# Optimization experiments

Hardware: AMD Instinct MI355X
Metric: run time of the kernel (lower is better)

Reference implementation:

```python
import jax, jax.numpy as jnp
import numpy as np
from jax import lax

B, T, D = 256, 512, 256          # batch, time, input_dim (neurons)
HE, HC, HG = 256, 256, 256       # encoder/controller/generator hidden
L, F = 64, 64                    # latent_dim, factor_dim


def gru_cell(x, h, Wih, Whh, bih, bhh):
    # PyTorch GRU gate order: r, z, n
    gi = x @ Wih.T + bih
    gh = h @ Whh.T + bhh
    ir, iz, inn = jnp.split(gi, 3, axis=-1)
    hr, hz, hn = jnp.split(gh, 3, axis=-1)
    r = jax.nn.sigmoid(ir + hr)
    z = jax.nn.sigmoid(iz + hz)
    n = jnp.tanh(inn + r * hn)
    return (1.0 - z) * n + z * h


def setup_inputs() -> dict:
    key = jax.random.key(0)
    ks = iter(jax.random.split(key, 40))
    def p(shape, scale=0.05):
        return (jax.random.normal(next(ks), shape, dtype=jnp.float32) * scale)
    inp = {
        "x": jax.random.normal(next(ks), (B, T, D), dtype=jnp.float32),
        "eps_u": jax.random.normal(next(ks), (T, B, L), dtype=jnp.float32),
        # bidirectional encoder GRU (forward / backward directions)
        "Wih_ef": p((3 * HE, D)), "Whh_ef": p((3 * HE, HE)), "bih_ef": p((3 * HE,)), "bhh_ef": p((3 * HE,)),
        "Wih_eb": p((3 * HE, D)), "Whh_eb": p((3 * HE, HE)), "bih_eb": p((3 * HE,)), "bhh_eb": p((3 * HE,)),
        # initial-condition heads
        "W_mu0": p((L, 2 * HE)), "b_mu0": p((L,)), "W_lv0": p((L, 2 * HE)), "b_lv0": p((L,)),
        # controller GRU + heads
        "Wih_c": p((3 * HC, D + F)), "Whh_c": p((3 * HC, HC)), "bih_c": p((3 * HC,)), "bhh_c": p((3 * HC,)),
        "W_cmu": p((L, HC)), "b_cmu": p((L,)), "W_clv": p((L, HC)), "b_clv": p((L,)),
        # generator GRU
        "Wih_g": p((3 * HG, L)), "Whh_g": p((3 * HG, HG)), "bih_g": p((3 * HG,)), "bhh_g": p((3 * HG,)),
        # readouts
        "W_f": p((F, HG)), "b_f": p((F,)), "W_r": p((D, F)), "b_r": p((D,)),
    }
    return inp


def reference(x, eps_u, Wih_ef, Whh_ef, bih_ef, bhh_ef, Wih_eb, Whh_eb, bih_eb, bhh_eb,
              W_mu0, b_mu0, W_lv0, b_lv0, Wih_c, Whh_c, bih_c, bhh_c,
              W_cmu, b_cmu, W_clv, b_clv, Wih_g, Whh_g, bih_g, bhh_g,
              W_f, b_f, W_r, b_r):
    xt = jnp.transpose(x, (1, 0, 2))  # [T, B, D]
    h0 = jnp.zeros((x.shape[0], HE), dtype=x.dtype)

    def enc_f(h, x_t):
        return gru_cell(x_t, h, Wih_ef, Whh_ef, bih_ef, bhh_ef), None

    def enc_b(h, x_t):
        return gru_cell(x_t, h, Wih_eb, Whh_eb, bih_eb, bhh_eb), None

    h_fwd, _ = lax.scan(enc_f, h0, xt)
    h_bwd, _ = lax.scan(enc_b, h0, xt, reverse=True)
    h_enc = jnp.concatenate([h_fwd, h_bwd], axis=-1)  # [B, 2*HE]

    mu0 = h_enc @ W_mu0.T + b_mu0
    lv0 = h_enc @ W_lv0.T + b_lv0
    kl_ics = (0.5 * jnp.sum(jnp.exp(lv0) + mu0 ** 2 - 1.0 - lv0, axis=1)).mean()
    # note: z0 is sampled in the original but never used (generator starts from zeros)

    c0 = jnp.zeros((x.shape[0], HC), dtype=x.dtype)
    g0 = jnp.zeros((x.shape[0], HG), dtype=x.dtype)
    f0 = jnp.zeros((x.shape[0], F), dtype=x.dtype)

    def step(carry, inputs):
        c_h, g_h, prev_f = carry
        x_t, eps_t = inputs
        c_in = jnp.concatenate([x_t, prev_f], axis=-1)  # [B, D+F]
        c_h = gru_cell(c_in, c_h, Wih_c, Whh_c, bih_c, bhh_c)
        mu_u = c_h @ W_cmu.T + b_cmu
        lv_u = c_h @ W_clv.T + b_clv
        u_t = mu_u + eps_t * jnp.exp(0.5 * lv_u)
        kl_t = (0.5 * jnp.sum(jnp.exp(lv_u) + mu_u ** 2 - 1.0 - lv_u, axis=1)).mean()
        g_h = gru_cell(u_t, g_h, Wih_g, Whh_g, bih_g, bhh_g)
        factors = g_h @ W_f.T + b_f
        rates_t = jnp.exp(factors @ W_r.T + b_r)
        return (c_h, g_h, factors), (rates_t, factors, kl_t)

    _, (rates, factors_all, kl_ts) = lax.scan(step, (c0, g0, f0), (xt, eps_u))
    rates = jnp.transpose(rates, (1, 0, 2))           # [B, T, D]
    factors_all = jnp.transpose(factors_all, (1, 0, 2))  # [B, T, F]
    kl_ctrl = kl_ts.mean()  # sum of per-step means / T
    return (rates, kl_ics, kl_ctrl, factors_all)
```

## Files before the change

### kernel.cpp

```cpp
#include <hip/hip_runtime.h>

typedef unsigned char u8;
typedef unsigned short u16;
typedef unsigned int u32;
typedef unsigned long long u64;
typedef short short8 __attribute__((ext_vector_type(8)));
typedef __bf16 bf16x8 __attribute__((ext_vector_type(8)));
typedef float f32x4 __attribute__((ext_vector_type(4)));
typedef float f32x2 __attribute__((ext_vector_type(2)));
typedef long longx2 __attribute__((ext_vector_type(2)));

#define DEV static __device__ __forceinline__

struct Params {
  const float *x, *eps;
  const float *Wih_ef, *Whh_ef, *bih_ef, *bhh_ef;
  const float *Wih_eb, *Whh_eb, *bih_eb, *bhh_eb;
  const float *W_mu0, *b_mu0, *W_lv0, *b_lv0;
  const float *Wih_c, *Whh_c, *bih_c, *bhh_c;
  const float *W_cmu, *b_cmu, *W_clv, *b_clv;
  const float *Wih_g, *Whh_g, *bih_g, *bhh_g;
  const float *W_f, *b_f, *W_r, *b_r;
  u8  *Xf8;
  u16 *ebf;
  u16 *wihcbf, *wihefbf, *wihebbf;
  float *bfc;
  float *bfe;
  u8 *wihef8, *whhef8, *wiheb8, *whheb8;
  u8 *whhc8, *whhg8;
  u8 *wihcf8, *wihg8;
  u8 *wf8, *wcmu8, *wclv8;
  u16 *wrbf;
  float *cbn;
  float *ebn;
  float *gb;
  float *hdb;
  float *fb2;
  float *eb;
  float *henc;
  float *klacc;
  float *klics;
  u8 *Gxc;
  u8 *Gxe;
  int useGxe;
  float *out;
};

constexpr size_t RATES_N = 33554432ull;
constexpr size_t FOUT    = RATES_N + 2ull;
constexpr size_t GXE_D   = 100663296ull;

DEV u16 f2bf(float x) {
  unsigned u = __builtin_bit_cast(unsigned, x);
  u = (u + 0x7FFFu + ((u >> 16) & 1u)) >> 16;
  return (u16)u;
}
DEV float bf2f(u32 s) { return __builtin_bit_cast(float, s << 16); }
DEV unsigned f2e4m3(float x) {
  unsigned u = __builtin_bit_cast(unsigned, x);
  unsigned s = (u >> 24) & 0x80u;
  float ax = __builtin_bit_cast(float, u & 0x7FFFFFFFu);
  if (ax > 448.f) return s | 0x7E;
  if (ax < 0.0009765625f) return s;
  if (ax < 0.015625f) {
    int m = (int)rintf(ax * 512.f);
    if (m >= 8) return s | 0x08;
    return s | (unsigned)m;
  }
  unsigned au = __builtin_bit_cast(unsigned, ax);
  int E = (int)(au >> 23) - 127;
  unsigned m = au & 0x7FFFFFu;
  unsigned r = (m + 0x7FFFFu + ((m >> 20) & 1u)) >> 20;
  if (r >= 8) { r = 0; ++E; if (E > 8) return s | 0x7E; }
  return s | ((unsigned)(E + 7) << 3) | r;
}
DEV float e4m3tof(unsigned b) {
  unsigned s = (b & 0x80u) << 24;
  unsigned e = (b >> 3) & 15u, m = b & 7u;
  float v;
  if (e) v = __builtin_bit_cast(float, ((e + 120u) << 23) | (m << 20));
  else   v = (float)m * 0.001953125f;
  return __builtin_bit_cast(float, __builtin_bit_cast(unsigned, v) | s);
}
template <bool HI>
DEV unsigned pk2fp8(float a, float b, unsigned old) {
#if __has_builtin(__builtin_amdgcn_cvt_pk_fp8_f32)
  return (unsigned)__builtin_amdgcn_cvt_pk_fp8_f32(a, b, (int)old, HI);
#else
  unsigned p = f2e4m3(a) | (f2e4m3(b) << 8);
  return HI ? ((old & 0xFFFFu) | (p << 16)) : ((old & 0xFFFF0000u) | p);
#endif
}
template <bool HI>
DEV f32x2 pkf32(unsigned w) {
#if __has_builtin(__builtin_amdgcn_cvt_pk_f32_fp8)
  return __builtin_amdgcn_cvt_pk_f32_fp8((int)w, HI);
#else
  unsigned h = HI ? (w >> 16) : w;
  f32x2 r; r[0] = e4m3tof(h & 255u); r[1] = e4m3tof((h >> 8) & 255u); return r;
#endif
}
DEV float sigm(float x) { return 1.f / (1.f + __expf(-x)); }
DEV float ftanh(float x) { float t = __expf(2.f * x); return 1.f - 2.f / (t + 1.f); }
DEV float gru_h(float pr, float pz, float pin, float phn, float hp) {
  float r = sigm(pr), z = sigm(pz);
  float n = ftanh(pin + r * phn);
  return (1.f - z) * n + z * hp;
}
DEV u64 pack8f8(const float* s) {
  u64 p = 0;
  #pragma unroll
  for (int e = 0; e < 8; ++e) p |= (u64)f2e4m3(s[e]) << (8 * e);
  return p;
}

DEV f32x4 MFMA(short8 a, short8 b, f32x4 c) {
  return __builtin_amdgcn_mfma_f32_16x16x32_bf16(
      __builtin_bit_cast(bf16x8, a), __builtin_bit_cast(bf16x8, b), c, 0, 0, 0);
}
DEV f32x4 mfma8(long a, long b, f32x4 c) {
  return __builtin_amdgcn_mfma_f32_16x16x32_fp8_fp8(a, b, c, 0, 0, 0);
}
DEV short8 ldfrag(const u16* p0, int stride) {
  const int l = threadIdx.x & 63;
  const u16* p = p0 + (size_t)(l & 15) * stride + ((l >> 4) << 3);
  return *reinterpret_cast<const short8*>(p);
}
DEV short8 ldfrag_f32(const float* p0, int stride) {
  const int l = threadIdx.x & 63;
  const float* p = p0 + (size_t)(l & 15) * stride + ((l >> 4) << 3);
  f32x4 a = *reinterpret_cast<const f32x4*>(p);
  f32x4 b = *reinterpret_cast<const f32x4*>(p + 4);
  short8 r;
  r[0]=(short)f2bf(a[0]); r[1]=(short)f2bf(a[1]); r[2]=(short)f2bf(a[2]); r[3]=(short)f2bf(a[3]);
  r[4]=(short)f2bf(b[0]); r[5]=(short)f2bf(b[1]); r[6]=(short)f2bf(b[2]); r[7]=(short)f2bf(b[3]);
  return r;
}
DEV longx2 ldws2(const u8* w, int tile, int p) {
  return *(const longx2*)(w + ((size_t)tile << 12) + (p << 10) + ((threadIdx.x & 63) << 4));
}
DEV longx2 ldws64x(const u8* w, int tile) {
  return *(const longx2*)(w + ((size_t)tile << 10) + ((threadIdx.x & 63) << 4));
}
DEV int fragoff(int row, int jb) { return jb * 128 + ((row ^ (jb & 15)) << 3); }
DEV long ldsF(const u8* m, int kk) {
  int l = threadIdx.x & 63;
  int jb = kk * 4 + (l >> 4);
  return *(const long*)(m + fragoff(l & 15, jb));
}
DEV long ldsF64(const u8* m, int k2) {
  int l = threadIdx.x & 63;
  int jb = k2 * 4 + (l >> 4);
  return *(const long*)(m + fragoff(l & 15, jb));
}
DEV void stF(u8* m, int row, int col, unsigned v) {
  *(unsigned*)(m + fragoff(row, col >> 3) + (col & 7)) = v;
}
DEV short8 ldsB16(const u8* m, int r0, int kk) {
  int l = threadIdx.x & 63;
  int row = r0 + (l & 15);
  int off = row * 512 + kk * 64 + ((l >> 4) << 4);
  off ^= (row & 7) << 4;
  return *(const short8*)(m + off);
}
DEV void stage16(u8* dst, const u8* src, int nbytes) {
  for (int i = threadIdx.x * 16; i < nbytes; i += blockDim.x * 16) {
    int row = i >> 9;
    int off = i ^ ((row & 7) << 4);
    *(f32x4*)(dst + off) = *(const f32x4*)(src + i);
  }
}
DEV void stageLin(u8* dst, const u8* src, int nbytes) {
  for (int i = threadIdx.x * 16; i < nbytes; i += 512 * 16)
    *(f32x4*)(dst + i) = *(const f32x4*)(src + i);
}

__global__ __launch_bounds__(256) void k_init(Params P) {
  const size_t g  = (size_t)blockIdx.x * 256 + threadIdx.x;
  const size_t gs = (size_t)gridDim.x * 256;
  if (!P.useGxe) {
    for (size_t i = g; i < 4194304ull; i += gs) {
      size_t flat = i << 3;
      int b = (int)(flat >> 17);
      int rem = (int)(flat & 131071);
      int t = rem >> 8, d = rem & 255;
      *(u64*)(P.Xf8 + (((size_t)t * 256 + b) << 8) + d) = pack8f8(P.x + flat);
    }
  }
  for (size_t o = g; o < 1048576ull; o += gs) {
    int l = (int)(o & 63), k2 = (int)((o >> 6) & 1);
    int bt = (int)((o >> 7) & 15), t = (int)(o >> 11);
    int row = bt * 16 + (l & 15), col = k2 * 32 + ((l >> 4) << 3);
    const float* s = P.eps + ((size_t)t * 256 + row) * 64 + col;
    f32x4 v0 = *(const f32x4*)s, v1 = *(const f32x4*)(s + 4);
    short8 ob;
    ob[0]=(short)f2bf(v0[0]); ob[1]=(short)f2bf(v0[1]); ob[2]=(short)f2bf(v0[2]); ob[3]=(short)f2bf(v0[3]);
    ob[4]=(short)f2bf(v1[0]); ob[5]=(short)f2bf(v1[1]); ob[6]=(short)f2bf(v1[2]); ob[7]=(short)f2bf(v1[3]);
    *(short8*)((u8*)P.ebf + o * 16) = ob;
  }
  const int gi = (int)g, gsi = (int)gs;
  for (int i = gi; i < 24576; i += gsi) {
    int l = i & 63, kk = (i >> 6) & 7, tile = i >> 9;
    int row = tile * 16 + (l & 15), col = kk * 32 + ((l >> 4) << 3);
    size_t so = (size_t)row * 256 + col;
    size_t db = ((size_t)tile << 12) + ((kk >> 1) << 10) + (l << 4) + ((kk & 1) << 3);
    *(u64*)(P.whhc8  + db) = pack8f8(P.Whh_c  + so);
    *(u64*)(P.whhg8  + db) = pack8f8(P.Whh_g  + so);
    *(u64*)(P.wihef8 + db) = pack8f8(P.Wih_ef + so);
    *(u64*)(P.whhef8 + db) = pack8f8(P.Whh_ef + so);
    *(u64*)(P.wiheb8 + db) = pack8f8(P.Wih_eb + so);
    *(u64*)(P.whheb8 + db) = pack8f8(P.Whh_eb + so);
  }
  for (int i = gi; i < 2048; i += gsi) {
    int l = i & 63, kk = (i >> 6) & 7, tile = i >> 9;
    int row = tile * 16 + (l & 15), col = kk * 32 + ((l >> 4) << 3);
    size_t so = (size_t)row * 256 + col;
    size_t db = ((size_t)tile << 12) + ((kk >> 1) << 10) + (l << 4) + ((kk & 1) << 3);
    *(u64*)(P.wf8   + db) = pack8f8(P.W_f   + so);
    *(u64*)(P.wcmu8 + db) = pack8f8(P.W_cmu + so);
    *(u64*)(P.wclv8 + db) = pack8f8(P.W_clv + so);
  }
  for (int i = gi; i < 6144; i += gsi) {
    int l = i & 63, k2 = (i >> 6) & 1, tile = i >> 7;
    int row = tile * 16 + (l & 15), col = k2 * 32 + ((l >> 4) << 3);
    size_t db = ((size_t)tile << 10) + (l << 4) + (k2 << 3);
    *(u64*)(P.wihcf8 + db) = pack8f8(P.Wih_c + (size_t)row * 320 + 256 + col);
    *(u64*)(P.wihg8  + db) = pack8f8(P.Wih_g + (size_t)row * 64 + col);
  }
  for (int i = gi; i < 196608; i += gsi) {
    int r = i >> 8, c = i & 255;
    P.wihcbf[i]  = f2bf(P.Wih_c[r * 320 + c]);
    P.wihefbf[i] = f2bf(P.Wih_ef[i]);
    P.wihebbf[i] = f2bf(P.Wih_eb[i]);
  }
  for (int i = gi; i < 16384; i += gsi) P.wrbf[i] = f2bf(P.W_r[i]);
  for (int i = gi; i < 768; i += gsi) {
    P.bfc[i] = P.bih_c[i] + (i < 512 ? P.bhh_c[i] : 0.f);
    P.bfe[i]       = P.bih_ef[i] + (i < 512 ? P.bhh_ef[i] : 0.f);
    P.bfe[768 + i] = P.bih_eb[i] + (i < 512 ? P.bhh_eb[i] : 0.f);
  }
  for (int i = gi; i < 256; i += gsi) {
    P.cbn[i] = P.bhh_c[512 + i];
    P.ebn[i]       = P.bhh_ef[512 + i];
    P.ebn[256 + i] = P.bhh_eb[512 + i];
    P.gb[i]        = P.bih_g[i] + P.bhh_g[i];
    P.gb[256 + i]  = P.bih_g[256 + i] + P.bhh_g[256 + i];
    P.gb[512 + i]  = P.bih_g[512 + i];
    P.gb[768 + i]  = P.bhh_g[512 + i];
    P.eb[i]        = P.bih_ef[i] + P.bhh_ef[i];
    P.eb[256 + i]  = P.bih_ef[256 + i] + P.bhh_ef[256 + i];
    P.eb[512 + i]  = P.bih_ef[512 + i];
    P.eb[768 + i]  = P.bhh_ef[512 + i];
    P.eb[1024 + i] = P.bih_eb[i] + P.bhh_eb[i];
    P.eb[1280 + i] = P.bih_eb[256 + i] + P.bhh_eb[256 + i];
    P.eb[1536 + i] = P.bih_eb[512 + i];
    P.eb[1792 + i] = P.bhh_eb[512 + i];
  }
  for (int i = gi; i < 128; i += gsi) P.hdb[i] = (i < 64) ? P.b_cmu[i] : P.b_clv[i - 64];
  for (int i = gi; i < 64; i += gsi)  P.fb2[i] = P.b_f[i];
}

__global__ __launch_bounds__(512, 2) void k_gx(Params P) {
  extern __shared__ char smem[];
  u8* sA = (u8*)smem;
  u8* sB = sA + 65536;
  const int nc = blockIdx.x % 6;
  const int tb = blockIdx.x / 6;
  const int t = tb >> 1, bh = tb & 1;
  for (int i = threadIdx.x * 8; i < 32768; i += 512 * 8) {
    int r = i >> 8, c = i & 255;
    const float* s = P.x + ((size_t)(bh * 128 + r) * 512 + t) * 256 + c;
    f32x4 v0 = *(const f32x4*)s, v1 = *(const f32x4*)(s + 4);
    short8 o;
    o[0]=(short)f2bf(v0[0]); o[1]=(short)f2bf(v0[1]); o[2]=(short)f2bf(v0[2]); o[3]=(short)f2bf(v0[3]);
    o[4]=(short)f2bf(v1[0]); o[5]=(short)f2bf(v1[1]); o[6]=(short)f2bf(v1[2]); o[7]=(short)f2bf(v1[3]);
    int off = (r * 512 + c * 2) ^ ((r & 7) << 4);
    *(short8*)(sB + off) = o;
  }
  const int lane = threadIdx.x & 63, wid = threadIdx.x >> 6;
  const int rq = (lane >> 4) << 2;
  const int nglob = nc * 128 + wid * 16;
  const int nmm = P.useGxe ? 3 : 1;
  #pragma unroll 1
  for (int mm = 0; mm < nmm; ++mm) {
    const u16* Abf = (mm == 0) ? P.wihcbf : ((mm == 1) ? P.wihefbf : P.wihebbf);
    const float* bias = (mm == 0) ? P.bfc : (P.bfe + (mm - 1) * 768);
    u8* dst = (mm == 0) ? P.Gxc : (P.Gxe + (size_t)(mm - 1) * GXE_D);
    stage16(sA, (const u8*)(Abf + (size_t)nc * 128 * 256), 65536);
    __syncthreads();
    short8 Af[8];
    #pragma unroll
    for (int kk = 0; kk < 8; ++kk) Af[kk] = ldsB16(sA, wid * 16, kk);
    float bq[4];
    #pragma unroll
    for (int q = 0; q < 4; ++q) bq[q] = bias[nglob + rq + q];
    #pragma unroll 1
    for (int bt = 0; bt < 8; ++bt) {
      f32x4 acc = {0.f, 0.f, 0.f, 0.f};
      #pragma unroll
      for (int kk = 0; kk < 8; ++kk)
        acc = MFMA(Af[kk], ldsB16(sB, bt * 16, kk), acc);
      float v0 = acc[0] + bq[0], v1 = acc[1] + bq[1], v2 = acc[2] + bq[2], v3 = acc[3] + bq[3];
      unsigned pw = pk2fp8<false>(v0, v1, 0u); pw = pk2fp8<true>(v2, v3, pw);
      *(u32*)(dst + (((size_t)(t * 16 + bh * 8 + bt) * 48 + (nglob >> 4)) << 8) + (lane << 2)) = pw;
    }
    __syncthreads();
  }
}

DEV void cg_role(const Params& P, int blk, char* smem) {
  u8* sWcf = (u8*)smem;
  u8* sWg  = sWcf + 49152;
  u8* sWhd = sWg + 49152;
  u8* hc8  = sWhd + 32768;
  u8* hg8  = hc8 + 8192;
  u8* f8b  = hg8 + 8192;
  float* sml  = (float*)(f8b + 2048);
  float* sred = sml + 16 * 132;

  const int lane = threadIdx.x & 63, wid = threadIdx.x >> 6;
  const int cl = lane & 15, rq = (lane >> 4) << 2;
  const int b0 = blk << 4, j0 = wid << 5, jt = wid << 1;
  const int sel = wid >> 2, l0 = (wid & 3) << 4;

  stageLin(sWcf, P.wihcf8, 49152);
  stageLin(sWg,  P.wihg8,  49152);
  stageLin(sWhd, P.wcmu8, 16384);
  stageLin(sWhd + 16384, P.wclv8, 16384);
  for (int i = threadIdx.x * 4; i < 18432; i += 512 * 4) *(int*)(hc8 + i) = 0;

  f32x4 bnv[2], brv[2], bzv[2], biv[2], bhv2[2];
  #pragma unroll
  for (int c2 = 0; c2 < 2; ++c2) {
    int j = j0 + c2 * 16 + rq;
    bnv[c2]  = *(const f32x4*)(P.cbn + j);
    brv[c2]  = *(const f32x4*)(P.gb + j);
    bzv[c2]  = *(const f32x4*)(P.gb + 256 + j);
    biv[c2]  = *(const f32x4*)(P.gb + 512 + j);
    bhv2[c2] = *(const f32x4*)(P.gb + 768 + j);
  }
  f32x4 hbv = *(const f32x4*)(P.hdb + sel * 64 + l0 + rq);
  f32x4 fbv = {0, 0, 0, 0};
  if (wid < 4) fbv = *(const f32x4*)(P.fb2 + (wid << 4) + rq);

  f32x4 hcM[2] = {{0,0,0,0},{0,0,0,0}};
  f32x4 hgM[2] = {{0,0,0,0},{0,0,0,0}};
  float klv = 0.f;
  __syncthreads();

  #pragma unroll 1
  for (int t = 0; t < 512; ++t) {
    const int cur = t & 1, prv = cur ^ 1;
    u8 *hcP = hc8 + prv * 4096, *hcC = hc8 + cur * 4096;
    u8 *hgP = hg8 + prv * 4096, *hgC = hg8 + cur * 4096;
    u32 gx[6];
    { const u8* gp = P.Gxc + (((size_t)(t * 16 + blk) * 48) << 8) + (lane << 2);
      #pragma unroll
      for (int c2 = 0; c2 < 2; ++c2)
        #pragma unroll
        for (int g3 = 0; g3 < 3; ++g3)
          gx[c2 * 3 + g3] = *(const u32*)(gp + ((g3 * 16 + jt + c2) << 8));
    }
    short8 ee0 = *(const short8*)((const u8*)P.ebf + (((size_t)(t * 16 + blk) * 2 + 0) << 10) + lane * 16);
    short8 ee1 = *(const short8*)((const u8*)P.ebf + (((size_t)(t * 16 + blk) * 2 + 1) << 10) + lane * 16);
    long hf[8];
    #pragma unroll
    for (int kk = 0; kk < 8; ++kk) hf[kk] = ldsF(hcP, kk);
    long ff0 = ldsF64(f8b + prv * 1024, 0);
    long ff1 = ldsF64(f8b + prv * 1024, 1);
    #pragma unroll
    for (int c2 = 0; c2 < 2; ++c2) {
      longx2 w0[4], w1[4], w2[4];
      #pragma unroll
      for (int p = 0; p < 4; ++p) {
        w0[p] = ldws2(P.whhc8,      jt + c2, p);
        w1[p] = ldws2(P.whhc8, 16 + jt + c2, p);
        w2[p] = ldws2(P.whhc8, 32 + jt + c2, p);
      }
      longx2 cf0 = ldws64x(sWcf,      jt + c2);
      longx2 cf1 = ldws64x(sWcf, 16 + jt + c2);
      longx2 cf2 = ldws64x(sWcf, 32 + jt + c2);
      f32x4 ar = {0,0,0,0}, az = {0,0,0,0}, ai = {0,0,0,0}, ah = {0,0,0,0};
      #pragma unroll
      for (int p = 0; p < 4; ++p) {
        ar = mfma8(w0[p].x, hf[2*p], ar);  ar = mfma8(w0[p].y, hf[2*p+1], ar);
        az = mfma8(w1[p].x, hf[2*p], az);  az = mfma8(w1[p].y, hf[2*p+1], az);
        ah = mfma8(w2[p].x, hf[2*p], ah);  ah = mfma8(w2[p].y, hf[2*p+1], ah);
      }
      ar = mfma8(cf0.x, ff0, ar); ar = mfma8(cf0.y, ff1, ar);
      az = mfma8(cf1.x, ff0, az); az = mfma8(cf1.y, ff1, az);
      ai = mfma8(cf2.x, ff0, ai); ai = mfma8(cf2.y, ff1, ai);
      f32x2 rlo = pkf32<false>(gx[c2*3+0]), rhi = pkf32<true>(gx[c2*3+0]);
      f32x2 zlo = pkf32<false>(gx[c2*3+1]), zhi = pkf32<true>(gx[c2*3+1]);
      f32x2 nlo = pkf32<false>(gx[c2*3+2]), nhi = pkf32<true>(gx[c2*3+2]);
      f32x4 bn = bnv[c2];
      float h0 = gru_h(ar[0]+rlo[0], az[0]+zlo[0], ai[0]+nlo[0], ah[0]+bn[0], hcM[c2][0]);
      float h1 = gru_h(ar[1]+rlo[1], az[1]+zlo[1], ai[1]+nlo[1], ah[1]+bn[1], hcM[c2][1]);
      float h2 = gru_h(ar[2]+rhi[0], az[2]+zhi[0], ai[2]+nhi[0], ah[2]+bn[2], hcM[c2][2]);
      float h3 = gru_h(ar[3]+rhi[1], az[3]+zhi[1], ai[3]+nhi[1], ah[3]+bn[3], hcM[c2][3]);
      hcM[c2][0] = h0; hcM[c2][1] = h1; hcM[c2][2] = h2; hcM[c2][3] = h3;
      unsigned pw = pk2fp8<false>(h0, h1, 0u); pw = pk2fp8<true>(h2, h3, pw);
      stF(hcC, cl, j0 + c2 * 16 + rq, pw);
    }
    longx2 pg0[4], pg1[4], pg2[4];
    #pragma unroll
    for (int p = 0; p < 4; ++p) {
      pg0[p] = ldws2(P.whhg8,      jt, p);
      pg1[p] = ldws2(P.whhg8, 16 + jt, p);
      pg2[p] = ldws2(P.whhg8, 32 + jt, p);
    }
    __syncthreads();
    { long hcv[8];
      #pragma unroll
      for (int kk = 0; kk < 8; ++kk) hcv[kk] = ldsF(hcC, kk);
      f32x4 am = {0,0,0,0};
      #pragma unroll
      for (int p = 0; p < 4; ++p) {
        longx2 wp = ldws2(sWhd + sel * 16384, wid & 3, p);
        am = mfma8(wp.x, hcv[2*p], am);
        am = mfma8(wp.y, hcv[2*p+1], am);
      }
      am += hbv;
      *(f32x4*)(sml + cl * 132 + sel * 64 + l0 + rq) = am;
    }
    __syncthreads();
    long U[2];
    { const float* ml = sml + cl * 132;
      const int kh = (lane >> 4) << 3;
      #pragma unroll
      for (int k2 = 0; k2 < 2; ++k2) {
        f32x4 mu0 = *(const f32x4*)(ml + k2 * 32 + kh);
        f32x4 mu1 = *(const f32x4*)(ml + k2 * 32 + kh + 4);
        f32x4 lv0 = *(const f32x4*)(ml + 64 + k2 * 32 + kh);
        f32x4 lv1 = *(const f32x4*)(ml + 64 + k2 * 32 + kh + 4);
        short8 ev = k2 ? ee1 : ee0;
        float uu[8];
        #pragma unroll
        for (int e = 0; e < 4; ++e) {
          float epv = bf2f((u32)(u16)ev[e]);
          uu[e] = mu0[e] + epv * __expf(0.5f * lv0[e]);
        }
        #pragma unroll
        for (int e = 0; e < 4; ++e) {
          float epv = bf2f((u32)(u16)ev[4 + e]);
          uu[4 + e] = mu1[e] + epv * __expf(0.5f * lv1[e]);
        }
        unsigned pa = pk2fp8<false>(uu[0], uu[1], 0u); pa = pk2fp8<true>(uu[2], uu[3], pa);
        unsigned pb = pk2fp8<false>(uu[4], uu[5], 0u); pb = pk2fp8<true>(uu[6], uu[7], pb);
        U[k2] = (long)(((u64)pb << 32) | (u64)pa);
      }
    }
    long hg[8];
    #pragma unroll
    for (int kk = 0; kk < 8; ++kk) hg[kk] = ldsF(hgP, kk);
    #pragma unroll
    for (int c2 = 0; c2 < 2; ++c2) {
      longx2 g0[4], g1[4], g2[4];
      if (c2 == 0) {
        #pragma unroll
        for (int p = 0; p < 4; ++p) { g0[p] = pg0[p]; g1[p] = pg1[p]; g2[p] = pg2[p]; }
      } else {
        #pragma unroll
        for (int p = 0; p < 4; ++p) {
          g0[p] = ldws2(P.whhg8,      jt + 1, p);
          g1[p] = ldws2(P.whhg8, 16 + jt + 1, p);
          g2[p] = ldws2(P.whhg8, 32 + jt + 1, p);
        }
      }
      longx2 u0 = ldws64x(sWg,      jt + c2);
      longx2 u1 = ldws64x(sWg, 16 + jt + c2);
      longx2 u2 = ldws64x(sWg, 32 + jt + c2);
      f32x4 gr = {0,0,0,0}, gz = {0,0,0,0}, gi = {0,0,0,0}, gh = {0,0,0,0};
      #pragma unroll
      for (int p = 0; p < 4; ++p) {
        gr = mfma8(g0[p].x, hg[2*p], gr);  gr = mfma8(g0[p].y, hg[2*p+1], gr);
        gz = mfma8(g1[p].x, hg[2*p], gz);  gz = mfma8(g1[p].y, hg[2*p+1], gz);
        gh = mfma8(g2[p].x, hg[2*p], gh);  gh = mfma8(g2[p].y, hg[2*p+1], gh);
      }
      gr = mfma8(u0.x, U[0], gr); gr = mfma8(u0.y, U[1], gr);
      gz = mfma8(u1.x, U[0], gz); gz = mfma8(u1.y, U[1], gz);
      gi = mfma8(u2.x, U[0], gi); gi = mfma8(u2.y, U[1], gi);
      float h0 = gru_h(gr[0]+brv[c2][0], gz[0]+bzv[c2][0], gi[0]+biv[c2][0], gh[0]+bhv2[c2][0], hgM[c2][0]);
      float h1 = gru_h(gr[1]+brv[c2][1], gz[1]+bzv[c2][1], gi[1]+biv[c2][1], gh[1]+bhv2[c2][1], hgM[c2][1]);
      float h2 = gru_h(gr[2]+brv[c2][2], gz[2]+bzv[c2][2], gi[2]+biv[c2][2], gh[2]+bhv2[c2][2], hgM[c2][2]);
      float h3 = gru_h(gr[3]+brv[c2][3], gz[3]+bzv[c2][3], gi[3]+biv[c2][3], gh[3]+bhv2[c2][3], hgM[c2][3]);
      hgM[c2][0] = h0; hgM[c2][1] = h1; hgM[c2][2] = h2; hgM[c2][3] = h3;
      unsigned pw = pk2fp8<false>(h0, h1, 0u); pw = pk2fp8<true>(h2, h3, pw);
      stF(hgC, cl, j0 + c2 * 16 + rq, pw);
    }
    __syncthreads();
    if (wid < 4) {
      long hgv[8];
      #pragma unroll
      for (int kk = 0; kk < 8; ++kk) hgv[kk] = ldsF(hgC, kk);
      f32x4 af = {0,0,0,0};
      #pragma unroll
      for (int p = 0; p < 4; ++p) {
        longx2 wp = ldws2(P.wf8, wid, p);
        af = mfma8(wp.x, hgv[2*p], af);
        af = mfma8(wp.y, hgv[2*p+1], af);
      }
      af += fbv;
      float* fo = P.out + FOUT + (size_t)(b0 + cl) * 32768 + (size_t)t * 64 + wid * 16 + rq;
      f32x2 lo = {af[0], af[1]}, hi2 = {af[2], af[3]};
      *(f32x2*)fo = lo;
      *(f32x2*)(fo + 2) = hi2;
      unsigned pw = pk2fp8<false>(af[0], af[1], 0u); pw = pk2fp8<true>(af[2], af[3], pw);
      stF(f8b + cur * 1024, cl, wid * 16 + rq, pw);
    } else {
      #pragma unroll
      for (int e = 0; e < 4; ++e) {
        int p = ((wid - 4) * 64 + lane) * 4 + e;
        int row = p >> 6, l = p & 63;
        float mu = sml[row * 132 + l], lv = sml[row * 132 + 64 + l];
        klv += __expf(lv) + mu * mu - 1.f - lv;
      }
    }
    __syncthreads();
  }
  if (wid >= 4) {
    float v = klv;
    v += __shfl_down(v, 32); v += __shfl_down(v, 16); v += __shfl_down(v, 8);
    v += __shfl_down(v, 4);  v += __shfl_down(v, 2);  v += __shfl_down(v, 1);
    if (lane == 0) sred[wid] = v;
  }
  __syncthreads();
  if (threadIdx.x == 0) P.klacc[blk] = sred[4] + sred[5] + sred[6] + sred[7];
}

template <bool GXE>
DEV void enc_role(const Params& P, int dir, int b0, char* smem) {
  u8* sWhh = (u8*)smem;
  u8* h8   = sWhh + 131072;
  u8* sx   = h8 + 8192;
  const int lane = threadIdx.x & 63, wid = threadIdx.x >> 6;
  const int cl = lane & 15, rq = (lane >> 4) << 2;
  const int j0 = wid << 5, jt = wid << 1;
  const int btile = b0 >> 4;
  const u8* wihG = dir ? P.wiheb8 : P.wihef8;
  const u8* whhG = dir ? P.whheb8 : P.whhef8;
  stageLin(sWhh, whhG, 131072);
  for (int i = threadIdx.x * 4; i < 8192; i += 512 * 4) *(int*)(h8 + i) = 0;
  f32x4 bnv[2], brv[2], bzv[2], biv[2], bhv2[2];
  #pragma unroll
  for (int c2 = 0; c2 < 2; ++c2) {
    int j = j0 + c2 * 16 + rq;
    if (GXE) {
      bnv[c2] = *(const f32x4*)(P.ebn + dir * 256 + j);
    } else {
      const float* ebt = P.eb + dir * 1024;
      brv[c2]  = *(const f32x4*)(ebt + j);
      bzv[c2]  = *(const f32x4*)(ebt + 256 + j);
      biv[c2]  = *(const f32x4*)(ebt + 512 + j);
      bhv2[c2] = *(const f32x4*)(ebt + 768 + j);
    }
  }
  f32x4 heM[2] = {{0,0,0,0},{0,0,0,0}};
  const int ssrc = threadIdx.x * 8;
  if (!GXE) {
    const int t0 = dir ? 511 : 0;
    *(u64*)(sx + fragoff(threadIdx.x >> 5, threadIdx.x & 31)) =
        *(const u64*)(P.Xf8 + (((size_t)t0 * 256 + b0) << 8) + ssrc);
  }
  __syncthreads();

  #pragma unroll 1
  for (int i = 0; i < 512; ++i) {
    const int cur = i & 1, prv = cur ^ 1;
    const int t = dir ? (511 - i) : i;
    u8 *hP = h8 + prv * 4096, *hC = h8 + cur * 4096;
    u32 gx[6];
    u64 xpre = 0;
    const u8* sxc = sx + cur * 4096;
    if (GXE) {
      const u8* gp = P.Gxe + (size_t)dir * GXE_D +
                     (((size_t)(t * 16 + btile) * 48) << 8) + (lane << 2);
      #pragma unroll
      for (int c2 = 0; c2 < 2; ++c2)
        #pragma unroll
        for (int g3 = 0; g3 < 3; ++g3)
          gx[c2 * 3 + g3] = *(const u32*)(gp + ((g3 * 16 + jt + c2) << 8));
    } else {
      if (i < 511) {
        int tn = dir ? (t - 1) : (t + 1);
        xpre = *(const u64*)(P.Xf8 + (((size_t)tn * 256 + b0) << 8) + ssrc);
      }
    }
    long hp[8];
    #pragma unroll
    for (int kk = 0; kk < 8; ++kk) hp[kk] = ldsF(hP, kk);
    #pragma unroll
    for (int c2 = 0; c2 < 2; ++c2) {
      longx2 Hr[4], Hz[4], Hn[4];
      #pragma unroll
      for (int p = 0; p < 4; ++p) {
        Hr[p] = ldws2(sWhh,      jt + c2, p);
        Hz[p] = ldws2(sWhh, 16 + jt + c2, p);
        Hn[p] = ldws2(whhG, 32 + jt + c2, p);
      }
      f32x4 er = {0,0,0,0}, ez = {0,0,0,0}, ei = {0,0,0,0}, eh = {0,0,0,0};
      #pragma unroll
      for (int p = 0; p < 4; ++p) {
        er = mfma8(Hr[p].x, hp[2*p], er);  er = mfma8(Hr[p].y, hp[2*p+1], er);
        ez = mfma8(Hz[p].x, hp[2*p], ez);  ez = mfma8(Hz[p].y, hp[2*p+1], ez);
        eh = mfma8(Hn[p].x, hp[2*p], eh);  eh = mfma8(Hn[p].y, hp[2*p+1], eh);
      }
      if (!GXE) {
        long xv[8];
        #pragma unroll
        for (int kk = 0; kk < 8; ++kk) xv[kk] = ldsF(sxc, kk);
        longx2 Ir[4], Iz[4], In[4];
        #pragma unroll
        for (int p = 0; p < 4; ++p) {
          Ir[p] = ldws2(wihG,      jt + c2, p);
          Iz[p] = ldws2(wihG, 16 + jt + c2, p);
          In[p] = ldws2(wihG, 32 + jt + c2, p);
        }
        #pragma unroll
        for (int p = 0; p < 4; ++p) {
          er = mfma8(Ir[p].x, xv[2*p], er);  er = mfma8(Ir[p].y, xv[2*p+1], er);
          ez = mfma8(Iz[p].x, xv[2*p], ez);  ez = mfma8(Iz[p].y, xv[2*p+1], ez);
          ei = mfma8(In[p].x, xv[2*p], ei);  ei = mfma8(In[p].y, xv[2*p+1], ei);
        }
      }
      float h0, h1, h2, h3;
      if (GXE) {
        f32x2 rlo = pkf32<false>(gx[c2*3+0]), rhi = pkf32<true>(gx[c2*3+0]);
        f32x2 zlo = pkf32<false>(gx[c2*3+1]), zhi = pkf32<true>(gx[c2*3+1]);
        f32x2 nlo = pkf32<false>(gx[c2*3+2]), nhi = pkf32<true>(gx[c2*3+2]);
        f32x4 bn = bnv[c2];
        h0 = gru_h(er[0]+rlo[0], ez[0]+zlo[0], nlo[0], eh[0]+bn[0], heM[c2][0]);
        h1 = gru_h(er[1]+rlo[1], ez[1]+zlo[1], nlo[1], eh[1]+bn[1], heM[c2][1]);
        h2 = gru_h(er[2]+rhi[0], ez[2]+zhi[0], nhi[0], eh[2]+bn[2], heM[c2][2]);
        h3 = gru_h(er[3]+rhi[1], ez[3]+zhi[1], nhi[1], eh[3]+bn[3], heM[c2][3]);
      } else {
        h0 = gru_h(er[0]+brv[c2][0], ez[0]+bzv[c2][0], ei[0]+biv[c2][0], eh[0]+bhv2[c2][0], heM[c2][0]);
        h1 = gru_h(er[1]+brv[c2][1], ez[1]+bzv[c2][1], ei[1]+biv[c2][1], eh[1]+bhv2[c2][1], heM[c2][1]);
        h2 = gru_h(er[2]+brv[c2][2], ez[2]+bzv[c2][2], ei[2]+biv[c2][2], eh[2]+bhv2[c2][2], heM[c2][2]);
        h3 = gru_h(er[3]+brv[c2][3], ez[3]+bzv[c2][3], ei[3]+biv[c2][3], eh[3]+bhv2[c2][3], heM[c2][3]);
      }
      heM[c2][0] = h0; heM[c2][1] = h1; heM[c2][2] = h2; heM[c2][3] = h3;
      unsigned pw = pk2fp8<false>(h0, h1, 0u); pw = pk2fp8<true>(h2, h3, pw);
      stF(hC, cl, j0 + c2 * 16 + rq, pw);
    }
    if (!GXE && i < 511)
      *(u64*)(sx + prv * 4096 + fragoff(threadIdx.x >> 5, threadIdx.x & 31)) = xpre;
    __syncthreads();
  }
  #pragma unroll
  for (int c2 = 0; c2 < 2; ++c2)
    *(f32x4*)(P.henc + (size_t)(dir * 256 + b0 + cl) * 256 + j0 + c2 * 16 + rq) = heM[c2];
}

__global__ __launch_bounds__(512)
__attribute__((amdgpu_waves_per_eu(2, 2)))
void k_main(Params P) {
  extern __shared__ char smem[];
  const int blk = blockIdx.x;
  if (blk < 16) cg_role(P, blk, smem);
  else {
    const int e = blk - 16;
    if (P.useGxe) enc_role<true>(P, e >> 4, (e & 15) << 4, smem);
    else          enc_role<false>(P, e >> 4, (e & 15) << 4, smem);
  }
}

__global__ __launch_bounds__(256) void k_post(Params P) {
  const int blk = blockIdx.x;
  if (blk < 32) {
    __shared__ float red[4];
    float ka = 0.f;
    #pragma unroll 1
    for (int pp = 0; pp < 2; ++pp) {
      int p = blk * 512 + threadIdx.x * 2 + pp;
      int b = p >> 6, l = p & 63;
      float mu = P.b_mu0[l], lv = P.b_lv0[l];
      const float* wm = P.W_mu0 + (size_t)l * 512;
      const float* wl = P.W_lv0 + (size_t)l * 512;
      const float* h0 = P.henc + (size_t)b * 256;
      const float* h1 = P.henc + (size_t)(256 + b) * 256;
      #pragma unroll 4
      for (int k = 0; k < 256; ++k) {
        float hf = h0[k], hb = h1[k];
        mu += hf * wm[k] + hb * wm[256 + k];
        lv += hf * wl[k] + hb * wl[256 + k];
      }
      ka += __expf(lv) + mu * mu - 1.f - lv;
    }
    const int lane = threadIdx.x & 63, wid = threadIdx.x >> 6;
    ka += __shfl_down(ka, 32); ka += __shfl_down(ka, 16); ka += __shfl_down(ka, 8);
    ka += __shfl_down(ka, 4);  ka += __shfl_down(ka, 2);  ka += __shfl_down(ka, 1);
    if (lane == 0) red[wid] = ka;
    __syncthreads();
    if (threadIdx.x == 0) P.klics[blk] = red[0] + red[1] + red[2] + red[3];
  } else {
    const int lane = threadIdx.x & 63, wid = threadIdx.x >> 6;
    const int cl = lane & 15, rq = (lane >> 4) << 2;
    const int gw = (blk - 32) * 4 + wid;
    const size_t r0 = (size_t)gw << 4;
    const float* Fs = P.out + FOUT;
    short8 F0 = ldfrag_f32(Fs + r0 * 64, 64);
    short8 F1 = ldfrag_f32(Fs + r0 * 64 + 32, 64);
    #pragma unroll 1
    for (int ct = 0; ct < 16; ++ct) {
      const int d0 = ct << 4;
      const u16* W = P.wrbf + (size_t)d0 * 64;
      f32x4 a = {0,0,0,0};
      a = MFMA(ldfrag(W, 64), F0, a);
      a = MFMA(ldfrag(W + 32, 64), F1, a);
      f32x4 rb = *(const f32x4*)(P.b_r + d0 + rq);
      f32x4 o;
      o[0] = __expf(a[0] + rb[0]); o[1] = __expf(a[1] + rb[1]);
      o[2] = __expf(a[2] + rb[2]); o[3] = __expf(a[3] + rb[3]);
      *(f32x4*)(P.out + (r0 + cl) * 256 + d0 + rq) = o;
    }
  }
}

__global__ void k_final(Params P) {
  if (threadIdx.x == 0) {
    float s = 0.f, s2 = 0.f;
    for (int i = 0; i < 16; ++i) s += P.klacc[i];
    for (int i = 0; i < 32; ++i) s2 += P.klics[i];
    P.out[RATES_N]     = s2 * (0.5f / 256.f);
    P.out[RATES_N + 1] = s  * (0.5f / (256.f * 512.f));
  }
}

extern "C" void kernel_launch(void* const* d_in, const int* in_sizes, int n_in,
                              void* d_out, int out_size, void* d_ws, size_t ws_size,
                              hipStream_t stream) {
  (void)in_sizes; (void)n_in; (void)out_size;
  Params P;
  const float* const* in = (const float* const*)d_in;
  P.x = in[0];      P.eps = in[1];
  P.Wih_ef = in[2]; P.Whh_ef = in[3]; P.bih_ef = in[4]; P.bhh_ef = in[5];
  P.Wih_eb = in[6]; P.Whh_eb = in[7]; P.bih_eb = in[8]; P.bhh_eb = in[9];
  P.W_mu0 = in[10]; P.b_mu0 = in[11]; P.W_lv0 = in[12]; P.b_lv0 = in[13];
  P.Wih_c = in[14]; P.Whh_c = in[15]; P.bih_c = in[16]; P.bhh_c = in[17];
  P.W_cmu = in[18]; P.b_cmu = in[19]; P.W_clv = in[20]; P.b_clv = in[21];
  P.Wih_g = in[22]; P.Whh_g = in[23]; P.bih_g = in[24]; P.bhh_g = in[25];
  P.W_f = in[26];   P.b_f = in[27];   P.W_r = in[28];   P.b_r = in[29];

  char* w = (char*)d_ws;
  size_t off = 0;
  auto take = [&](size_t bytes) -> char* {
    char* r = w + off;
    off = (off + bytes + 255) & ~(size_t)255;
    return r;
  };
  P.Xf8     = (u8*)take(33554432ull);
  P.ebf     = (u16*)take(16777216ull * 2);
  P.wihcbf  = (u16*)take(196608ull * 2);
  P.wihefbf = (u16*)take(196608ull * 2);
  P.wihebbf = (u16*)take(196608ull * 2);
  P.bfc     = (float*)take(768ull * 4);
  P.bfe     = (float*)take(1536ull * 4);
  P.wihef8  = (u8*)take(196608ull);
  P.whhef8  = (u8*)take(196608ull);
  P.wiheb8  = (u8*)take(196608ull);
  P.whheb8  = (u8*)take(196608ull);
  P.whhc8   = (u8*)take(196608ull);
  P.whhg8   = (u8*)take(196608ull);
  P.wihcf8  = (u8*)take(49152ull);
  P.wihg8   = (u8*)take(49152ull);
  P.wf8     = (u8*)take(16384ull);
  P.wcmu8   = (u8*)take(16384ull);
  P.wclv8   = (u8*)take(16384ull);
  P.wrbf    = (u16*)take(16384ull * 2);
  P.cbn     = (float*)take(256ull * 4);
  P.ebn     = (float*)take(512ull * 4);
  P.gb      = (float*)take(1024ull * 4);
  P.hdb     = (float*)take(128ull * 4);
  P.fb2     = (float*)take(64ull * 4);
  P.eb      = (float*)take(2048ull * 4);
  P.henc    = (float*)take(131072ull * 4);
  P.klacc   = (float*)take(64ull * 4);
  P.klics   = (float*)take(64ull * 4);
  size_t gxe_off = (off + 255) & ~(size_t)255;
  P.useGxe = (gxe_off + 2 * GXE_D <= ws_size) ? 1 : 0;
  P.Gxe = P.useGxe ? (u8*)(w + gxe_off) : (u8*)w;
  P.Gxc = (u8*)d_out;
  P.out = (float*)d_out;

  hipLaunchKernelGGL(k_init,  dim3(2048), dim3(256), 0, stream, P);
  hipLaunchKernelGGL(k_gx,    dim3(6144), dim3(512), 131072, stream, P);
  hipLaunchKernelGGL(k_main,  dim3(48),   dim3(512), 158016, stream, P);
  hipLaunchKernelGGL(k_post,  dim3(2080), dim3(256), 0, stream, P);
  hipLaunchKernelGGL(k_final, dim3(1),    dim3(64),  0, stream, P);
}
```

Measured before the change: 4.644 ms.

## Fold factor readout into controller input weights to drop per-step sync

Precomputes Wih_c[:,256:] @ W_f (and its bias term) so the controller GRU consumes the previous generator hidden state directly instead of the previous factors. The factors buffer in shared memory and the trailing barrier in the recurrent loop go away, which shortens the serial per-step dependency chain. In exchange the controller does a K=256 fp8 matmul against a 196KB global weight instead of a K=64 matmul from shared memory, and the fused product is quantized to fp8, which changes rounding.

```diff
diff --git a/kernel.cpp b/kernel.cpp
--- a/kernel.cpp
+++ b/kernel.cpp
@@ -28,9 +28,11 @@
   float *bfe;
   u8 *wihef8, *whhef8, *wiheb8, *whheb8;
   u8 *whhc8, *whhg8;
-  u8 *wihcf8, *wihg8;
+  u8 *wcomb8;
+  u8 *wihg8;
   u8 *wf8, *wcmu8, *wclv8;
   u16 *wrbf;
+  float *foldc;
   float *cbn;
   float *ebn;
   float *gb;
@@ -148,11 +150,6 @@
   int jb = kk * 4 + (l >> 4);
   return *(const long*)(m + fragoff(l & 15, jb));
 }
-DEV long ldsF64(const u8* m, int k2) {
-  int l = threadIdx.x & 63;
-  int jb = k2 * 4 + (l >> 4);
-  return *(const long*)(m + fragoff(l & 15, jb));
-}
 DEV void stF(u8* m, int row, int col, unsigned v) {
   *(unsigned*)(m + fragoff(row, col >> 3) + (col & 7)) = v;
 }
@@ -211,6 +208,24 @@
     *(u64*)(P.wiheb8 + db) = pack8f8(P.Wih_eb + so);
     *(u64*)(P.whheb8 + db) = pack8f8(P.Whh_eb + so);
   }
+  for (int i = gi; i < 196608; i += gsi) {
+    int r = i >> 8, c = i & 255;
+    float acc = 0.f;
+    const float* wr = P.Wih_c + (size_t)r * 320 + 256;
+    #pragma unroll 4
+    for (int l = 0; l < 64; ++l) acc += wr[l] * P.W_f[l * 256 + c];
+    int tile = r >> 4, row15 = r & 15;
+    int kk = c >> 5, lh = (c >> 3) & 3, e = c & 7;
+    int lane = lh * 16 + row15;
+    size_t db = ((size_t)tile << 12) + ((size_t)(kk >> 1) << 10) + (lane << 4) + ((kk & 1) << 3) + e;
+    P.wcomb8[db] = (u8)f2e4m3(acc);
+  }
+  for (int i = gi; i < 768; i += gsi) {
+    float acc = 0.f;
+    const float* wr = P.Wih_c + (size_t)i * 320 + 256;
+    for (int l = 0; l < 64; ++l) acc += wr[l] * P.b_f[l];
+    P.foldc[i] = acc;
+  }
   for (int i = gi; i < 2048; i += gsi) {
     int l = i & 63, kk = (i >> 6) & 7, tile = i >> 9;
     int row = tile * 16 + (l & 15), col = kk * 32 + ((l >> 4) << 3);
@@ -224,7 +239,6 @@
     int l = i & 63, k2 = (i >> 6) & 1, tile = i >> 7;
     int row = tile * 16 + (l & 15), col = k2 * 32 + ((l >> 4) << 3);
     size_t db = ((size_t)tile << 10) + (l << 4) + (k2 << 3);
-    *(u64*)(P.wihcf8 + db) = pack8f8(P.Wih_c + (size_t)row * 320 + 256 + col);
     *(u64*)(P.wihg8  + db) = pack8f8(P.Wih_g + (size_t)row * 64 + col);
   }
   for (int i = gi; i < 196608; i += gsi) {
@@ -309,13 +323,11 @@
 }
 
 DEV void cg_role(const Params& P, int blk, char* smem) {
-  u8* sWcf = (u8*)smem;
-  u8* sWg  = sWcf + 49152;
+  u8* sWg  = (u8*)smem;
   u8* sWhd = sWg + 49152;
   u8* hc8  = sWhd + 32768;
   u8* hg8  = hc8 + 8192;
-  u8* f8b  = hg8 + 8192;
-  float* sml  = (float*)(f8b + 2048);
+  float* sml  = (float*)(hg8 + 8192);
   float* sred = sml + 16 * 132;
 
   const int lane = threadIdx.x & 63, wid = threadIdx.x >> 6;
@@ -323,13 +335,13 @@
   const int b0 = blk << 4, j0 = wid << 5, jt = wid << 1;
   const int sel = wid >> 2, l0 = (wid & 3) << 4;
 
-  stageLin(sWcf, P.wihcf8, 49152);
   stageLin(sWg,  P.wihg8,  49152);
   stageLin(sWhd, P.wcmu8, 16384);
   stageLin(sWhd + 16384, P.wclv8, 16384);
-  for (int i = threadIdx.x * 4; i < 18432; i += 512 * 4) *(int*)(hc8 + i) = 0;
+  for (int i = threadIdx.x * 4; i < 16384; i += 512 * 4) *(int*)(hc8 + i) = 0;
 
   f32x4 bnv[2], brv[2], bzv[2], biv[2], bhv2[2];
+  f32x4 frv[2], fzv[2], fnv[2];
   #pragma unroll
   for (int c2 = 0; c2 < 2; ++c2) {
     int j = j0 + c2 * 16 + rq;
@@ -338,6 +350,9 @@
     bzv[c2]  = *(const f32x4*)(P.gb + 256 + j);
     biv[c2]  = *(const f32x4*)(P.gb + 512 + j);
     bhv2[c2] = *(const f32x4*)(P.gb + 768 + j);
+    frv[c2]  = *(const f32x4*)(P.foldc + j);
+    fzv[c2]  = *(const f32x4*)(P.foldc + 256 + j);
+    fnv[c2]  = *(const f32x4*)(P.foldc + 512 + j);
   }
   f32x4 hbv = *(const f32x4*)(P.hdb + sel * 64 + l0 + rq);
   f32x4 fbv = {0, 0, 0, 0};
@@ -353,6 +368,7 @@
     const int cur = t & 1, prv = cur ^ 1;
     u8 *hcP = hc8 + prv * 4096, *hcC = hc8 + cur * 4096;
     u8 *hgP = hg8 + prv * 4096, *hgC = hg8 + cur * 4096;
+    const float sc = (t == 0) ? 0.f : 1.f;
     u32 gx[6];
     { const u8* gp = P.Gxc + (((size_t)(t * 16 + blk) * 48) << 8) + (lane << 2);
       #pragma unroll
@@ -363,11 +379,9 @@
     }
     short8 ee0 = *(const short8*)((const u8*)P.ebf + (((size_t)(t * 16 + blk) * 2 + 0) << 10) + lane * 16);
     short8 ee1 = *(const short8*)((const u8*)P.ebf + (((size_t)(t * 16 + blk) * 2 + 1) << 10) + lane * 16);
-    long hf[8];
+    long hf[8], hgv[8];
     #pragma unroll
-    for (int kk = 0; kk < 8; ++kk) hf[kk] = ldsF(hcP, kk);
-    long ff0 = ldsF64(f8b + prv * 1024, 0);
-    long ff1 = ldsF64(f8b + prv * 1024, 1);
+    for (int kk = 0; kk < 8; ++kk) { hf[kk] = ldsF(hcP, kk); hgv[kk] = ldsF(hgP, kk); }
     #pragma unroll
     for (int c2 = 0; c2 < 2; ++c2) {
       longx2 w0[4], w1[4], w2[4];
@@ -377,27 +391,35 @@
         w1[p] = ldws2(P.whhc8, 16 + jt + c2, p);
         w2[p] = ldws2(P.whhc8, 32 + jt + c2, p);
       }
-      longx2 cf0 = ldws64x(sWcf,      jt + c2);
-      longx2 cf1 = ldws64x(sWcf, 16 + jt + c2);
-      longx2 cf2 = ldws64x(sWcf, 32 + jt + c2);
+      longx2 m0[4], m1[4], m2[4];
+      #pragma unroll
+      for (int p = 0; p < 4; ++p) {
+        m0[p] = ldws2(P.wcomb8,      jt + c2, p);
+        m1[p] = ldws2(P.wcomb8, 16 + jt + c2, p);
+        m2[p] = ldws2(P.wcomb8, 32 + jt + c2, p);
+      }
       f32x4 ar = {0,0,0,0}, az = {0,0,0,0}, ai = {0,0,0,0}, ah = {0,0,0,0};
       #pragma unroll
       for (int p = 0; p < 4; ++p) {
         ar = mfma8(w0[p].x, hf[2*p], ar);  ar = mfma8(w0[p].y, hf[2*p+1], ar);
         az = mfma8(w1[p].x, hf[2*p], az);  az = mfma8(w1[p].y, hf[2*p+1], az);
         ah = mfma8(w2[p].x, hf[2*p], ah);  ah = mfma8(w2[p].y, hf[2*p+1], ah);
-      }
-      ar = mfma8(cf0.x, ff0, ar); ar = mfma8(cf0.y, ff1, ar);
-      az = mfma8(cf1.x, ff0, az); az = mfma8(cf1.y, ff1, az);
-      ai = mfma8(cf2.x, ff0, ai); ai = mfma8(cf2.y, ff1, ai);
+        ar = mfma8(m0[p].x, hgv[2*p], ar); ar = mfma8(m0[p].y, hgv[2*p+1], ar);
+        az = mfma8(m1[p].x, hgv[2*p], az); az = mfma8(m1[p].y, hgv[2*p+1], az);
+        ai = mfma8(m2[p].x, hgv[2*p], ai); ai = mfma8(m2[p].y, hgv[2*p+1], ai);
+      }
       f32x2 rlo = pkf32<false>(gx[c2*3+0]), rhi = pkf32<true>(gx[c2*3+0]);
       f32x2 zlo = pkf32<false>(gx[c2*3+1]), zhi = pkf32<true>(gx[c2*3+1]);
       f32x2 nlo = pkf32<false>(gx[c2*3+2]), nhi = pkf32<true>(gx[c2*3+2]);
       f32x4 bn = bnv[c2];
-      float h0 = gru_h(ar[0]+rlo[0], az[0]+zlo[0], ai[0]+nlo[0], ah[0]+bn[0], hcM[c2][0]);
-      float h1 = gru_h(ar[1]+rlo[1], az[1]+zlo[1], ai[1]+nlo[1], ah[1]+bn[1], hcM[c2][1]);
-      float h2 = gru_h(ar[2]+rhi[0], az[2]+zhi[0], ai[2]+nhi[0], ah[2]+bn[2], hcM[c2][2]);
-      float h3 = gru_h(ar[3]+rhi[1], az[3]+zhi[1], ai[3]+nhi[1], ah[3]+bn[3], hcM[c2][3]);
+      float h0 = gru_h(ar[0]+rlo[0]+sc*frv[c2][0], az[0]+zlo[0]+sc*fzv[c2][0],
+                       ai[0]+nlo[0]+sc*fnv[c2][0], ah[0]+bn[0], hcM[c2][0]);
+      float h1 = gru_h(ar[1]+rlo[1]+sc*frv[c2][1], az[1]+zlo[1]+sc*fzv[c2][1],
+                       ai[1]+nlo[1]+sc*fnv[c2][1], ah[1]+bn[1], hcM[c2][1]);
+      float h2 = gru_h(ar[2]+rhi[0]+sc*frv[c2][2], az[2]+zhi[0]+sc*fzv[c2][2],
+                       ai[2]+nhi[0]+sc*fnv[c2][2], ah[2]+bn[2], hcM[c2][2]);
+      float h3 = gru_h(ar[3]+rhi[1]+sc*frv[c2][3], az[3]+zhi[1]+sc*fzv[c2][3],
+                       ai[3]+nhi[1]+sc*fnv[c2][3], ah[3]+bn[3], hcM[c2][3]);
       hcM[c2][0] = h0; hcM[c2][1] = h1; hcM[c2][2] = h2; hcM[c2][3] = h3;
       unsigned pw = pk2fp8<false>(h0, h1, 0u); pw = pk2fp8<true>(h2, h3, pw);
       stF(hcC, cl, j0 + c2 * 16 + rq, pw);
@@ -490,23 +512,21 @@
     }
     __syncthreads();
     if (wid < 4) {
-      long hgv[8];
-      #pragma unroll
-      for (int kk = 0; kk < 8; ++kk) hgv[kk] = ldsF(hgC, kk);
+      long hgv2[8];
+      #pragma unroll
+      for (int kk = 0; kk < 8; ++kk) hgv2[kk] = ldsF(hgC, kk);
       f32x4 af = {0,0,0,0};
       #pragma unroll
       for (int p = 0; p < 4; ++p) {
         longx2 wp = ldws2(P.wf8, wid, p);
-        af = mfma8(wp.x, hgv[2*p], af);
-        af = mfma8(wp.y, hgv[2*p+1], af);
+        af = mfma8(wp.x, hgv2[2*p], af);
+        af = mfma8(wp.y, hgv2[2*p+1], af);
       }
       af += fbv;
       float* fo = P.out + FOUT + (size_t)(b0 + cl) * 32768 + (size_t)t * 64 + wid * 16 + rq;
       f32x2 lo = {af[0], af[1]}, hi2 = {af[2], af[3]};
       *(f32x2*)fo = lo;
       *(f32x2*)(fo + 2) = hi2;
-      unsigned pw = pk2fp8<false>(af[0], af[1], 0u); pw = pk2fp8<true>(af[2], af[3], pw);
-      stF(f8b + cur * 1024, cl, wid * 16 + rq, pw);
     } else {
       #pragma unroll
       for (int e = 0; e < 4; ++e) {
@@ -516,7 +536,6 @@
         klv += __expf(lv) + mu * mu - 1.f - lv;
       }
     }
-    __syncthreads();
   }
   if (wid >= 4) {
     float v = klv;
@@ -762,12 +781,13 @@
   P.whheb8  = (u8*)take(196608ull);
   P.whhc8   = (u8*)take(196608ull);
   P.whhg8   = (u8*)take(196608ull);
-  P.wihcf8  = (u8*)take(49152ull);
+  P.wcomb8  = (u8*)take(196608ull);
   P.wihg8   = (u8*)take(49152ull);
   P.wf8     = (u8*)take(16384ull);
   P.wcmu8   = (u8*)take(16384ull);
   P.wclv8   = (u8*)take(16384ull);
   P.wrbf    = (u16*)take(16384ull * 2);
+  P.foldc   = (float*)take(768ull * 4);
   P.cbn     = (float*)take(256ull * 4);
   P.ebn     = (float*)take(512ull * 4);
   P.gb      = (float*)take(1024ull * 4);
@@ -785,7 +805,7 @@
 
   hipLaunchKernelGGL(k_init,  dim3(2048), dim3(256), 0, stream, P);
   hipLaunchKernelGGL(k_gx,    dim3(6144), dim3(512), 131072, stream, P);
-  hipLaunchKernelGGL(k_main,  dim3(48),   dim3(512), 158016, stream, P);
+  hipLaunchKernelGGL(k_main,  dim3(48),   dim3(512), 147456, stream, P);
   hipLaunchKernelGGL(k_post,  dim3(2080), dim3(256), 0, stream, P);
   hipLaunchKernelGGL(k_final, dim3(1),    dim3(64),  0, stream, P);
 }
```

Measured after the change: 5.865 ms. 1.26x slower.
